# Performance work log

Hardware: AMD Instinct MI355X
Metric: run time of the kernel (lower is better)

Reference implementation:

```python
import jax, jax.numpy as jnp
import numpy as np

B, C, H, E, V = 64, 200, 1024, 1024, 50257
NEG_INF = -100000.0


def setup_inputs() -> dict:
    key = jax.random.key(0)
    ks = jax.random.split(key, 16)
    p = 1.0 / np.sqrt(H)
    inp = {
        "input": jax.random.normal(ks[0], (B, 1, E), jnp.float32),
        "hidden": jax.random.normal(ks[1], (1, B, H), jnp.float32),
        "list_context_hidden": jax.random.normal(ks[2], (C, B, H), jnp.float32),
        "context_hiddens": jax.random.normal(ks[3], (B, C, H), jnp.float32),
        "topic_vector": jax.random.normal(ks[4], (B, 1, H), jnp.float32),
        "pad_matrix": jax.random.randint(ks[5], (B, C), 0, 2) > 0,
        # attention params
        "dyna_W": jax.random.normal(ks[6], (H, H), jnp.float32) * p,
        "dyna_U": jax.random.normal(ks[7], (H, H), jnp.float32) * p,
        "dyna_v": jax.random.normal(ks[8], (H, 1), jnp.float32) * p,
        # GRU params (torch layout: W_ih (3H, in), W_hh (3H, H))
        "W_ih": jax.random.normal(ks[9], (3 * H, 2 * H + E), jnp.float32) * p,
        "W_hh": jax.random.normal(ks[10], (3 * H, H), jnp.float32) * p,
        "b_ih": jax.random.normal(ks[11], (3 * H,), jnp.float32) * p,
        "b_hh": jax.random.normal(ks[12], (3 * H,), jnp.float32) * p,
        # output projection
        "W_out": jax.random.normal(ks[13], (V, H), jnp.float32) * p,
        "b_out": jax.random.normal(ks[14], (V,), jnp.float32) * p,
    }
    return inp


def _gru_step(x, h, W_ih, W_hh, b_ih, b_hh):
    # x: (B, in), h: (B, H) -> h': (B, H); torch GRUCell math
    gi = x @ W_ih.T + b_ih            # (B, 3H)
    gh = h @ W_hh.T + b_hh            # (B, 3H)
    r = jax.nn.sigmoid(gi[:, :H] + gh[:, :H])
    z = jax.nn.sigmoid(gi[:, H:2 * H] + gh[:, H:2 * H])
    n = jnp.tanh(gi[:, 2 * H:] + r * gh[:, 2 * H:])
    return (1.0 - z) * n + z * h


def reference(input, hidden, list_context_hidden, context_hiddens, topic_vector,
              pad_matrix, dyna_W, dyna_U, dyna_v, W_ih, W_hh, b_ih, b_hh,
              W_out, b_out):
    h0 = hidden[0]                                         # (B, H)
    # additive attention, vectorized over the C contexts
    q = h0 @ dyna_W                                        # (B, H)
    k = jnp.einsum('cbh,hk->cbk', list_context_hidden, dyna_U)  # (C, B, H)
    scores = jnp.tanh(q[None, :, :] + k) @ dyna_v          # (C, B, 1)
    scores = scores[..., 0].T                              # (B, C)
    scores = jnp.where(pad_matrix, NEG_INF, scores)
    attn = jax.nn.softmax(scores, axis=1)                  # (B, C)
    applied = jnp.einsum('bc,bch->bh', attn, context_hiddens)  # (B, H)
    # GRU over a single step
    x = jnp.concatenate([input[:, 0], topic_vector[:, 0], applied], axis=1)  # (B, E+2H)
    h_new = _gru_step(x, h0, W_ih, W_hh, b_ih, b_hh)       # (B, H)
    logits = h_new @ W_out.T + b_out                       # (B, V)
    out = jax.nn.log_softmax(logits, axis=1)
    return out, h_new[None]
```

## Files before the change

### kernel.cpp

```cpp
#include <hip/hip_runtime.h>
#include <hip/hip_bf16.h>
#include <math.h>

constexpr int Bsz = 64, Cctx = 200, Hdim = 1024, Vv = 50257;
constexpr float NEG_INF_V = -100000.0f;

typedef __attribute__((ext_vector_type(8))) short s16x8;
typedef __attribute__((ext_vector_type(4))) float fx4;
typedef unsigned int u32;

__device__ __forceinline__ unsigned short f2bf(float f) {
  unsigned int u = __builtin_bit_cast(unsigned int, f);
  unsigned int r = (u + 0x7fffu + ((u >> 16) & 1u)) >> 16;
  return (unsigned short)r;
}

__device__ __forceinline__ float fast_tanh(float x) {
  float e2 = __expf(2.f * x);
  return 1.f - 2.f / (e2 + 1.f);
}

__device__ __forceinline__ void gl_lds16(const unsigned short* g, unsigned short* l) {
  __builtin_amdgcn_global_load_lds(
      (const __attribute__((address_space(1))) u32*)g,
      (__attribute__((address_space(3))) u32*)l, 16, 0, 0);
}

__global__ __launch_bounds__(256)
void gemm_att(const unsigned short* __restrict__ Ab, const unsigned short* __restrict__ Bb,
              const float* __restrict__ qmat, const float* __restrict__ vvec,
              float* __restrict__ scores) {
  __shared__ unsigned short As[2][128 * 64];
  __shared__ unsigned short Bs[2][128 * 64];
  int f = blockIdx.x + blockIdx.y * 8;
  int xcd = f & 7, jj = f >> 3;
  int my = xcd + 8 * (jj % 13), mx = jj / 13;
  if (my >= 100) return;
  const int bm0 = my * 128, bn0 = mx * 128;
  const int tid = threadIdx.x, lane = tid & 63, wid = tid >> 6;
  const int wm0 = (wid >> 1) * 64, wn0 = (wid & 1) * 64;
  const int ar = lane & 15;
  const int q4 = lane >> 4;
  const int sw = ar & 7;

  auto STAGE = [&](int buf, int kt) {
    #pragma unroll
    for (int i = 0; i < 4; ++i) {
      int s = tid + i * 256;
      int row = s >> 3;
      int sc = ((s & 7) ^ (row & 7)) * 8;
      gl_lds16(&Ab[(size_t)(bm0 + row) * Hdim + kt + sc], &As[buf][s * 8]);
    }
    #pragma unroll
    for (int i = 0; i < 4; ++i) {
      int s = tid + i * 256;
      int row = s >> 3;
      int sc = ((s & 7) ^ (row & 7)) * 8;
      gl_lds16(&Bb[(size_t)(bn0 + row) * Hdim + kt + sc], &Bs[buf][s * 8]);
    }
  };

  fx4 acc[4][4] = {};
  int buf = 0;
  STAGE(0, 0);
  __syncthreads();

  for (int t = 0; t < 16; ++t) {
    if (t < 15) STAGE(buf ^ 1, (t + 1) * 64);
    asm volatile("" ::: "memory");
    #pragma unroll
    for (int kk = 0; kk < 2; ++kk) {
      s16x8 a[4], b[4];
      #pragma unroll
      for (int i = 0; i < 4; ++i)
        a[i] = *reinterpret_cast<const s16x8*>(
            &As[buf][(wm0 + i * 16 + ar) * 64 + (((kk * 4 + q4) ^ sw) * 8)]);
      #pragma unroll
      for (int j2 = 0; j2 < 4; ++j2)
        b[j2] = *reinterpret_cast<const s16x8*>(
            &Bs[buf][(wn0 + j2 * 16 + ar) * 64 + (((kk * 4 + q4) ^ sw) * 8)]);
      #pragma unroll
      for (int i = 0; i < 4; ++i)
        #pragma unroll
        for (int j2 = 0; j2 < 4; ++j2)
          acc[i][j2] = __builtin_amdgcn_mfma_f32_16x16x32_bf16(a[i], b[j2], acc[i][j2], 0, 0, 0);
    }
    __syncthreads();
    buf ^= 1;
  }

  const int rg = q4 * 4, cg = ar;
  #pragma unroll
  for (int i = 0; i < 4; ++i) {
    #pragma unroll
    for (int p = 0; p < 4; ++p) {
      int mg = bm0 + wm0 + i * 16 + rg + p;
      int brow = mg & 63;
      float rs = 0.f;
      #pragma unroll
      for (int j2 = 0; j2 < 4; ++j2) {
        int ng = bn0 + wn0 + j2 * 16 + cg;
        float t = fast_tanh(acc[i][j2][p] + qmat[brow * Hdim + ng]);
        rs += t * vvec[ng];
      }
      rs += __shfl_xor(rs, 1); rs += __shfl_xor(rs, 2);
      rs += __shfl_xor(rs, 4); rs += __shfl_xor(rs, 8);
      if (cg == 0) atomicAdd(&scores[brow * Cctx + (mg >> 6)], rs);
    }
  }
}

__device__ __forceinline__ void stream_body(const unsigned short* ap, const float* bp,
                                            int K, fx4 acc[4]) {
  float4 b0 = *reinterpret_cast<const float4*>(bp);
  float4 b1 = *reinterpret_cast<const float4*>(bp + 4);
  float4 b2 = *reinterpret_cast<const float4*>(bp + 32);
  float4 b3 = *reinterpret_cast<const float4*>(bp + 36);
  for (int kt = 0; kt < K; kt += 64) {
    float4 c0 = b0, c1 = b1, c2 = b2, c3 = b3;
    if (kt + 64 < K) {
      b0 = *reinterpret_cast<const float4*>(bp + kt + 64);
      b1 = *reinterpret_cast<const float4*>(bp + kt + 68);
      b2 = *reinterpret_cast<const float4*>(bp + kt + 96);
      b3 = *reinterpret_cast<const float4*>(bp + kt + 100);
    }
    s16x8 bf0, bf1;
    bf0[0] = (short)f2bf(c0.x); bf0[1] = (short)f2bf(c0.y);
    bf0[2] = (short)f2bf(c0.z); bf0[3] = (short)f2bf(c0.w);
    bf0[4] = (short)f2bf(c1.x); bf0[5] = (short)f2bf(c1.y);
    bf0[6] = (short)f2bf(c1.z); bf0[7] = (short)f2bf(c1.w);
    bf1[0] = (short)f2bf(c2.x); bf1[1] = (short)f2bf(c2.y);
    bf1[2] = (short)f2bf(c2.z); bf1[3] = (short)f2bf(c2.w);
    bf1[4] = (short)f2bf(c3.x); bf1[5] = (short)f2bf(c3.y);
    bf1[6] = (short)f2bf(c3.z); bf1[7] = (short)f2bf(c3.w);
    #pragma unroll
    for (int i = 0; i < 4; ++i) {
      s16x8 af = *reinterpret_cast<const s16x8*>(ap + (size_t)i * 16 * K + kt);
      acc[i] = __builtin_amdgcn_mfma_f32_16x16x32_bf16(af, bf0, acc[i], 0, 0, 0);
    }
    #pragma unroll
    for (int i = 0; i < 4; ++i) {
      s16x8 af = *reinterpret_cast<const s16x8*>(ap + (size_t)i * 16 * K + kt + 32);
      acc[i] = __builtin_amdgcn_mfma_f32_16x16x32_bf16(af, bf1, acc[i], 0, 0, 0);
    }
  }
}

template<int EPI>
__global__ __launch_bounds__(64)
void stream_gemm(const unsigned short* __restrict__ Ab,
                 const float* __restrict__ Bm, int N, int K,
                 const float* __restrict__ bias, float* __restrict__ Cout) {
  const int lane = threadIdx.x;
  const int n0 = blockIdx.x * 16;
  const int c = lane & 15, qq = lane >> 4;
  const int brow = min(n0 + c, N - 1);
  fx4 acc[4] = {};
  stream_body(Ab + (size_t)c * K + qq * 8, Bm + (size_t)brow * K + qq * 8, K, acc);
  const int n = n0 + c;
  if (n < N) {
    float bv = (EPI == 2) ? bias[n] : 0.f;
    #pragma unroll
    for (int i = 0; i < 4; ++i)
      #pragma unroll
      for (int p = 0; p < 4; ++p)
        Cout[(size_t)(i * 16 + qq * 4 + p) * N + n] = acc[i][p] + bv;
  }
}

__global__ __launch_bounds__(64)
void qgh_gemm(const unsigned short* __restrict__ h0b, const float* __restrict__ Wt,
              const float* __restrict__ Whh, const float* __restrict__ bhh,
              float* __restrict__ q, float* __restrict__ gh) {
  const int lane = threadIdx.x;
  const int gw = blockIdx.x;
  const bool isq = gw < 64;
  const int n0 = isq ? gw * 16 : (gw - 64) * 16;
  const int N = isq ? 1024 : 3072;
  const float* B = isq ? Wt : Whh;
  const int c = lane & 15, qq = lane >> 4;
  fx4 acc[4] = {};
  stream_body(h0b + (size_t)c * 1024 + qq * 8, B + (size_t)(n0 + c) * 1024 + qq * 8, 1024, acc);
  const int n = n0 + c;
  float bv = isq ? 0.f : bhh[n];
  float* C = isq ? q : gh;
  #pragma unroll
  for (int i = 0; i < 4; ++i)
    #pragma unroll
    for (int p = 0; p < 4; ++p)
      C[(size_t)(i * 16 + qq * 4 + p) * N + n] = acc[i][p] + bv;
}

__global__ __launch_bounds__(64)
void gi_split(const unsigned short* __restrict__ xb, const float* __restrict__ Wih,
              float* __restrict__ part) {
  const int lane = threadIdx.x;
  const int t = blockIdx.x;
  const int w = blockIdx.y;
  const int c = lane & 15, qq = lane >> 4;
  constexpr int K = 3072, CH = 768;
  const float* bp = Wih + (size_t)(t * 16 + c) * K + w * CH + qq * 8;
  const unsigned short* ap = xb + (size_t)c * K + w * CH + qq * 8;
  fx4 acc[4] = {};
  float4 b0 = *reinterpret_cast<const float4*>(bp);
  float4 b1 = *reinterpret_cast<const float4*>(bp + 4);
  float4 b2 = *reinterpret_cast<const float4*>(bp + 32);
  float4 b3 = *reinterpret_cast<const float4*>(bp + 36);
  for (int kt = 0; kt < CH; kt += 64) {
    float4 c0 = b0, c1 = b1, c2 = b2, c3 = b3;
    if (kt + 64 < CH) {
      b0 = *reinterpret_cast<const float4*>(bp + kt + 64);
      b1 = *reinterpret_cast<const float4*>(bp + kt + 68);
      b2 = *reinterpret_cast<const float4*>(bp + kt + 96);
      b3 = *reinterpret_cast<const float4*>(bp + kt + 100);
    }
    s16x8 bf0, bf1;
    bf0[0] = (short)f2bf(c0.x); bf0[1] = (short)f2bf(c0.y);
    bf0[2] = (short)f2bf(c0.z); bf0[3] = (short)f2bf(c0.w);
    bf0[4] = (short)f2bf(c1.x); bf0[5] = (short)f2bf(c1.y);
    bf0[6] = (short)f2bf(c1.z); bf0[7] = (short)f2bf(c1.w);
    bf1[0] = (short)f2bf(c2.x); bf1[1] = (short)f2bf(c2.y);
    bf1[2] = (short)f2bf(c2.z); bf1[3] = (short)f2bf(c2.w);
    bf1[4] = (short)f2bf(c3.x); bf1[5] = (short)f2bf(c3.y);
    bf1[6] = (short)f2bf(c3.z); bf1[7] = (short)f2bf(c3.w);
    #pragma unroll
    for (int i = 0; i < 4; ++i) {
      s16x8 af = *reinterpret_cast<const s16x8*>(ap + (size_t)i * 16 * K + kt);
      acc[i] = __builtin_amdgcn_mfma_f32_16x16x32_bf16(af, bf0, acc[i], 0, 0, 0);
    }
    #pragma unroll
    for (int i = 0; i < 4; ++i) {
      s16x8 af = *reinterpret_cast<const s16x8*>(ap + (size_t)i * 16 * K + kt + 32);
      acc[i] = __builtin_amdgcn_mfma_f32_16x16x32_bf16(af, bf1, acc[i], 0, 0, 0);
    }
  }
  float* po = part + (size_t)w * 64 * 3072;
  const int n = t * 16 + c;
  #pragma unroll
  for (int i = 0; i < 4; ++i)
    #pragma unroll
    for (int p = 0; p < 4; ++p)
      po[(size_t)(i * 16 + qq * 4 + p) * 3072 + n] = acc[i][p];
}

__global__ __launch_bounds__(256)
void prep(const float* __restrict__ dW, const float* __restrict__ dU,
          const float* __restrict__ h0, float* __restrict__ Wt,
          unsigned short* __restrict__ ub, unsigned short* __restrict__ h0b) {
  const int z = blockIdx.z;
  const int tx = threadIdx.x & 31, ty = threadIdx.x >> 5;
  if (z < 2) {
    __shared__ float t[32][33];
    const float* in = z ? dU : dW;
    int bx = blockIdx.x * 32, by = blockIdx.y * 32;
    #pragma unroll
    for (int r = 0; r < 32; r += 8) t[ty + r][tx] = in[(size_t)(by + ty + r) * 1024 + bx + tx];
    __syncthreads();
    if (z == 0) {
      #pragma unroll
      for (int r = 0; r < 32; r += 8) Wt[(size_t)(bx + ty + r) * 1024 + by + tx] = t[tx][ty + r];
    } else {
      #pragma unroll
      for (int r = 0; r < 32; r += 8) ub[(size_t)(bx + ty + r) * 1024 + by + tx] = f2bf(t[tx][ty + r]);
    }
  } else {
    if (blockIdx.y) return;
    size_t i = (size_t)(blockIdx.x * 256 + threadIdx.x) * 8;
    float4 a = *reinterpret_cast<const float4*>(h0 + i);
    float4 b = *reinterpret_cast<const float4*>(h0 + i + 4);
    s16x8 h;
    h[0] = (short)f2bf(a.x); h[1] = (short)f2bf(a.y); h[2] = (short)f2bf(a.z); h[3] = (short)f2bf(a.w);
    h[4] = (short)f2bf(b.x); h[5] = (short)f2bf(b.y); h[6] = (short)f2bf(b.z); h[7] = (short)f2bf(b.w);
    *reinterpret_cast<s16x8*>(h0b + i) = h;
  }
}

__global__ void conv_bf16(const float* __restrict__ in, unsigned short* __restrict__ out) {
  size_t i = (size_t)(blockIdx.x * 256 + threadIdx.x) * 8;
  float4 a = *reinterpret_cast<const float4*>(in + i);
  float4 b = *reinterpret_cast<const float4*>(in + i + 4);
  s16x8 h;
  h[0] = (short)f2bf(a.x); h[1] = (short)f2bf(a.y); h[2] = (short)f2bf(a.z); h[3] = (short)f2bf(a.w);
  h[4] = (short)f2bf(b.x); h[5] = (short)f2bf(b.y); h[6] = (short)f2bf(b.z); h[7] = (short)f2bf(b.w);
  *reinterpret_cast<s16x8*>(out + i) = h;
}

__global__ __launch_bounds__(256)
void softmax_applied(const float* __restrict__ scores, const int* __restrict__ pad,
                     const float* __restrict__ ch, float* __restrict__ part) {
  const int g = blockIdx.x, b = blockIdx.y, t = threadIdx.x;
  const int lane = t & 63, w = t >> 6;
  __shared__ float at[256];
  __shared__ float red[8];
  float sv = 0.f, v = -3.4e38f;
  if (t < Cctx) { sv = pad[b * Cctx + t] ? NEG_INF_V : scores[b * Cctx + t]; v = sv; }
  #pragma unroll
  for (int o = 1; o < 64; o <<= 1) v = fmaxf(v, __shfl_xor(v, o));
  if (lane == 0) red[w] = v;
  __syncthreads();
  float m = fmaxf(fmaxf(red[0], red[1]), fmaxf(red[2], red[3]));
  float e = (t < Cctx) ? expf(sv - m) : 0.f;
  float s = e;
  #pragma unroll
  for (int o = 1; o < 64; o <<= 1) s += __shfl_xor(s, o);
  if (lane == 0) red[4 + w] = s;
  __syncthreads();
  float tot = red[4] + red[5] + red[6] + red[7];
  at[t] = e / tot;
  __syncthreads();
  const int h = t * 4;
  float4 a4 = make_float4(0.f, 0.f, 0.f, 0.f);
  for (int c2 = g * 25; c2 < g * 25 + 25; ++c2) {
    float a = at[c2];
    float4 vv = *reinterpret_cast<const float4*>(&ch[((size_t)b * Cctx + c2) * Hdim + h]);
    a4.x += a * vv.x; a4.y += a * vv.y; a4.z += a * vv.z; a4.w += a * vv.w;
  }
  *reinterpret_cast<float4*>(&part[((size_t)b * 8 + g) * Hdim + h]) = a4;
}

__global__ void build_xb(const float* __restrict__ inp, const float* __restrict__ topic,
                         const float* __restrict__ part, unsigned short* __restrict__ xb) {
  int j = blockIdx.x * 256 + threadIdx.x;
  int b = blockIdx.y;
  float v;
  if (j < 1024) v = inp[b * 1024 + j];
  else if (j < 2048) v = topic[b * 1024 + (j - 1024)];
  else {
    const float* pp = &part[(size_t)b * 8 * Hdim + (j - 2048)];
    v = 0.f;
    #pragma unroll
    for (int g = 0; g < 8; ++g) v += pp[g * Hdim];
  }
  xb[(size_t)b * 3072 + j] = f2bf(v);
}

__global__ void gru_gate(const float* __restrict__ pgi, const float* __restrict__ bih,
                         const float* __restrict__ gh, const float* __restrict__ h0,
                         float* __restrict__ out_h, unsigned short* __restrict__ hnb) {
  int idx = blockIdx.x * 256 + threadIdx.x;
  int b = idx >> 10, j = idx & 1023;
  float gr = bih[j], gz = bih[1024 + j], gn = bih[2048 + j];
  const float* pb = pgi + (size_t)b * 3072;
  #pragma unroll
  for (int w = 0; w < 4; ++w) {
    const float* pw = pb + (size_t)w * 64 * 3072;
    gr += pw[j]; gz += pw[1024 + j]; gn += pw[2048 + j];
  }
  const float* ghb = gh + (size_t)b * 3072;
  float r = 1.f / (1.f + expf(-(gr + ghb[j])));
  float z = 1.f / (1.f + expf(-(gz + ghb[1024 + j])));
  float n = tanhf(gn + r * ghb[2048 + j]);
  float h = (1.f - z) * n + z * h0[idx];
  out_h[idx] = h;
  hnb[idx] = f2bf(h);
}

__global__ __launch_bounds__(1024)
void lse_fused(float* __restrict__ out) {
  const int b = blockIdx.x, t = threadIdx.x, lane = t & 63, w = t >> 6;
  __shared__ float red[16];
  float* row = out + (size_t)b * Vv;
  float m = -3.4e38f;
  for (int i = t; i < Vv; i += 1024) m = fmaxf(m, row[i]);
  #pragma unroll
  for (int o = 1; o < 64; o <<= 1) m = fmaxf(m, __shfl_xor(m, o));
  if (lane == 0) red[w] = m;
  __syncthreads();
  float mm = red[0];
  #pragma unroll
  for (int k = 1; k < 16; ++k) mm = fmaxf(mm, red[k]);
  float s = 0.f;
  for (int i = t; i < Vv; i += 1024) s += expf(row[i] - mm);
  #pragma unroll
  for (int o = 1; o < 64; o <<= 1) s += __shfl_xor(s, o);
  __syncthreads();
  if (lane == 0) red[w] = s;
  __syncthreads();
  float ss = 0.f;
  #pragma unroll
  for (int k = 0; k < 16; ++k) ss += red[k];
  float lse = mm + logf(ss);
  for (int i = t; i < Vv; i += 1024) row[i] -= lse;
}

extern "C" void kernel_launch(void* const* d_in, const int* in_sizes, int n_in,
                              void* d_out, int out_size, void* d_ws, size_t ws_size,
                              hipStream_t stream) {
  const float* input  = (const float*)d_in[0];
  const float* hidden = (const float*)d_in[1];
  const float* lch    = (const float*)d_in[2];
  const float* ch     = (const float*)d_in[3];
  const float* topic  = (const float*)d_in[4];
  const int*   pad    = (const int*)d_in[5];
  const float* dyna_W = (const float*)d_in[6];
  const float* dyna_U = (const float*)d_in[7];
  const float* dyna_v = (const float*)d_in[8];
  const float* W_ih   = (const float*)d_in[9];
  const float* W_hh   = (const float*)d_in[10];
  const float* b_ih   = (const float*)d_in[11];
  const float* b_hh   = (const float*)d_in[12];
  const float* W_out  = (const float*)d_in[13];
  const float* b_out  = (const float*)d_in[14];

  float* out   = (float*)d_out;
  float* out_h = out + (size_t)Bsz * Vv;

  float* p = (float*)d_ws;
  float* Wt      = p; p += 1024 * 1024;
  float* q       = p; p += Bsz * Hdim;
  float* scores  = p; p += Bsz * Cctx;
  float* part_ap = p; p += Bsz * 8 * Hdim;
  float* gh      = p; p += Bsz * 3072;
  float* part_gi = p; p += 4 * Bsz * 3072;
  unsigned short* up = (unsigned short*)p;
  unsigned short* ub  = up; up += 1024 * 1024;
  unsigned short* lb  = up; up += (size_t)Cctx * Bsz * Hdim;
  unsigned short* h0b = up; up += Bsz * Hdim;
  unsigned short* hnb = up; up += Bsz * Hdim;
  unsigned short* xb  = up; up += Bsz * 3072;

  prep<<<dim3(32, 32, 3), 256, 0, stream>>>(dyna_W, dyna_U, hidden, Wt, ub, h0b);
  conv_bf16<<<(Cctx * Bsz * Hdim) / 2048, 256, 0, stream>>>(lch, lb);
  hipMemsetAsync(scores, 0, Bsz * Cctx * sizeof(float), stream);

  qgh_gemm<<<256, 64, 0, stream>>>(h0b, Wt, W_hh, b_hh, q, gh);

  gemm_att<<<dim3(8, 104), 256, 0, stream>>>(lb, ub, q, dyna_v, scores);

  softmax_applied<<<dim3(8, Bsz), 256, 0, stream>>>(scores, pad, ch, part_ap);
  build_xb<<<dim3(12, Bsz), 256, 0, stream>>>(input, topic, part_ap, xb);

  gi_split<<<dim3(192, 4), 64, 0, stream>>>(xb, W_ih, part_gi);

  gru_gate<<<(Bsz * Hdim) / 256, 256, 0, stream>>>(part_gi, b_ih, gh, hidden, out_h, hnb);

  stream_gemm<2><<<(Vv + 15) / 16, 64, 0, stream>>>(hnb, W_out, Vv, Hdim, b_out, out);

  lse_fused<<<Bsz, 1024, 0, stream>>>(out);
}
```

Before: 247.6 us.

## Load attention B operand directly from global, drop atomics for partial score buffer

The attention GEMM stops staging the dyna_U bf16 tile in LDS and has each lane read its B fragments straight from global memory (L2-resident, reused across blocks). This halves shared memory use, which together with launch_bounds(256,3) is meant to raise occupancy. Score accumulation switches from atomicAdd into a zeroed buffer to per-column-block partial writes that softmax_applied sums, removing the memset and the atomics. The risk is that direct global B loads are uncoalesced and expose latency inside the MFMA loop.

```diff
diff --git a/kernel.cpp b/kernel.cpp
--- a/kernel.cpp
+++ b/kernel.cpp
@@ -26,12 +26,11 @@
       (__attribute__((address_space(3))) u32*)l, 16, 0, 0);
 }
 
-__global__ __launch_bounds__(256)
+__global__ __launch_bounds__(256, 3)
 void gemm_att(const unsigned short* __restrict__ Ab, const unsigned short* __restrict__ Bb,
               const float* __restrict__ qmat, const float* __restrict__ vvec,
-              float* __restrict__ scores) {
+              float* __restrict__ part_sc) {
   __shared__ unsigned short As[2][128 * 64];
-  __shared__ unsigned short Bs[2][128 * 64];
   int f = blockIdx.x + blockIdx.y * 8;
   int xcd = f & 7, jj = f >> 3;
   int my = xcd + 8 * (jj % 13), mx = jj / 13;
@@ -39,9 +38,13 @@
   const int bm0 = my * 128, bn0 = mx * 128;
   const int tid = threadIdx.x, lane = tid & 63, wid = tid >> 6;
   const int wm0 = (wid >> 1) * 64, wn0 = (wid & 1) * 64;
-  const int ar = lane & 15;
-  const int q4 = lane >> 4;
+  const int ar = lane & 15, q4 = lane >> 4;
   const int sw = ar & 7;
+
+  const unsigned short* bptr[4];
+  #pragma unroll
+  for (int j2 = 0; j2 < 4; ++j2)
+    bptr[j2] = Bb + (size_t)(bn0 + wn0 + j2 * 16 + ar) * Hdim + q4 * 8;
 
   auto STAGE = [&](int buf, int kt) {
     #pragma unroll
@@ -51,19 +54,12 @@
       int sc = ((s & 7) ^ (row & 7)) * 8;
       gl_lds16(&Ab[(size_t)(bm0 + row) * Hdim + kt + sc], &As[buf][s * 8]);
     }
-    #pragma unroll
-    for (int i = 0; i < 4; ++i) {
-      int s = tid + i * 256;
-      int row = s >> 3;
-      int sc = ((s & 7) ^ (row & 7)) * 8;
-      gl_lds16(&Bb[(size_t)(bn0 + row) * Hdim + kt + sc], &Bs[buf][s * 8]);
-    }
   };
 
   fx4 acc[4][4] = {};
+  STAGE(0, 0);
+  __syncthreads();
   int buf = 0;
-  STAGE(0, 0);
-  __syncthreads();
 
   for (int t = 0; t < 16; ++t) {
     if (t < 15) STAGE(buf ^ 1, (t + 1) * 64);
@@ -72,13 +68,12 @@
     for (int kk = 0; kk < 2; ++kk) {
       s16x8 a[4], b[4];
       #pragma unroll
+      for (int j2 = 0; j2 < 4; ++j2)
+        b[j2] = *reinterpret_cast<const s16x8*>(bptr[j2] + t * 64 + kk * 32);
+      #pragma unroll
       for (int i = 0; i < 4; ++i)
         a[i] = *reinterpret_cast<const s16x8*>(
             &As[buf][(wm0 + i * 16 + ar) * 64 + (((kk * 4 + q4) ^ sw) * 8)]);
-      #pragma unroll
-      for (int j2 = 0; j2 < 4; ++j2)
-        b[j2] = *reinterpret_cast<const s16x8*>(
-            &Bs[buf][(wn0 + j2 * 16 + ar) * 64 + (((kk * 4 + q4) ^ sw) * 8)]);
       #pragma unroll
       for (int i = 0; i < 4; ++i)
         #pragma unroll
@@ -105,7 +100,7 @@
       }
       rs += __shfl_xor(rs, 1); rs += __shfl_xor(rs, 2);
       rs += __shfl_xor(rs, 4); rs += __shfl_xor(rs, 8);
-      if (cg == 0) atomicAdd(&scores[brow * Cctx + (mg >> 6)], rs);
+      if (cg == 0) part_sc[mx * 12800 + brow * Cctx + (mg >> 6)] = rs;
     }
   }
 }
@@ -286,14 +281,20 @@
 }
 
 __global__ __launch_bounds__(256)
-void softmax_applied(const float* __restrict__ scores, const int* __restrict__ pad,
+void softmax_applied(const float* __restrict__ part_sc, const int* __restrict__ pad,
                      const float* __restrict__ ch, float* __restrict__ part) {
   const int g = blockIdx.x, b = blockIdx.y, t = threadIdx.x;
   const int lane = t & 63, w = t >> 6;
   __shared__ float at[256];
   __shared__ float red[8];
   float sv = 0.f, v = -3.4e38f;
-  if (t < Cctx) { sv = pad[b * Cctx + t] ? NEG_INF_V : scores[b * Cctx + t]; v = sv; }
+  if (t < Cctx) {
+    float s8 = 0.f;
+    #pragma unroll
+    for (int mx = 0; mx < 8; ++mx) s8 += part_sc[mx * 12800 + b * Cctx + t];
+    sv = pad[b * Cctx + t] ? NEG_INF_V : s8;
+    v = sv;
+  }
   #pragma unroll
   for (int o = 1; o < 64; o <<= 1) v = fmaxf(v, __shfl_xor(v, o));
   if (lane == 0) red[w] = v;
@@ -408,7 +409,7 @@
   float* p = (float*)d_ws;
   float* Wt      = p; p += 1024 * 1024;
   float* q       = p; p += Bsz * Hdim;
-  float* scores  = p; p += Bsz * Cctx;
+  float* part_sc = p; p += 8 * Bsz * Cctx;
   float* part_ap = p; p += Bsz * 8 * Hdim;
   float* gh      = p; p += Bsz * 3072;
   float* part_gi = p; p += 4 * Bsz * 3072;
@@ -421,13 +422,12 @@
 
   prep<<<dim3(32, 32, 3), 256, 0, stream>>>(dyna_W, dyna_U, hidden, Wt, ub, h0b);
   conv_bf16<<<(Cctx * Bsz * Hdim) / 2048, 256, 0, stream>>>(lch, lb);
-  hipMemsetAsync(scores, 0, Bsz * Cctx * sizeof(float), stream);
 
   qgh_gemm<<<256, 64, 0, stream>>>(h0b, Wt, W_hh, b_hh, q, gh);
 
-  gemm_att<<<dim3(8, 104), 256, 0, stream>>>(lb, ub, q, dyna_v, scores);
-
-  softmax_applied<<<dim3(8, Bsz), 256, 0, stream>>>(scores, pad, ch, part_ap);
+  gemm_att<<<dim3(8, 104), 256, 0, stream>>>(lb, ub, q, dyna_v, part_sc);
+
+  softmax_applied<<<dim3(8, Bsz), 256, 0, stream>>>(part_sc, pad, ch, part_ap);
   build_xb<<<dim3(12, Bsz), 256, 0, stream>>>(input, topic, part_ap, xb);
 
   gi_split<<<dim3(192, 4), 64, 0, stream>>>(xb, W_ih, part_gi);
```

Measured after the change: 271.4 us. 1.1x slower.
